# Performance work log

Hardware: AMD Instinct MI355X
Metric: run time of the kernel (lower is better)

Reference implementation:

```python
import jax, jax.numpy as jnp
import numpy as np

N_NODES = 100000
NEG_SLOPE = 0.2  # PyG GATConv default


def gat_conv(x, src, dst, W, a_src, a_dst, n_nodes):
    """One PyG-style GATConv (with self-loops already appended to src/dst).
    x: [N, Fin], W: [Fin, H*C], a_src/a_dst: [H, C]. Returns [N, H, C]."""
    H, C = a_src.shape
    h = (x @ W).reshape(-1, H, C)                      # [N, H, C]
    s_src = jnp.einsum('nhc,hc->nh', h, a_src)         # [N, H]
    s_dst = jnp.einsum('nhc,hc->nh', h, a_dst)         # [N, H]
    e = jax.nn.leaky_relu(s_src[src] + s_dst[dst], NEG_SLOPE)  # [E, H]
    # segment softmax over incoming edges of each destination node
    e_max = jax.ops.segment_max(e, dst, num_segments=n_nodes)  # [N, H]
    e_exp = jnp.exp(e - e_max[dst])
    denom = jax.ops.segment_sum(e_exp, dst, num_segments=n_nodes)
    alpha = e_exp / (denom[dst] + 1e-16)               # [E, H]
    msg = h[src] * alpha[:, :, None]                   # [E, H, C]
    return jax.ops.segment_sum(msg, dst, num_segments=n_nodes)  # [N, H, C]


def setup_inputs() -> dict:
    key = jax.random.key(0)
    ks = jax.random.split(key, 10)
    in_dim, hidden, heads, out_dim = 128, 32, 4, 32
    N, E = N_NODES, 1600000
    x = jax.random.normal(ks[0], (N, in_dim), dtype=jnp.float32)
    edge_index = jax.random.randint(ks[1], (2, E), 0, N, dtype=jnp.int64)
    s = 0.1
    return {
        'x': x,
        'edge_index': edge_index,
        'W1': s * jax.random.normal(ks[2], (in_dim, heads * hidden), dtype=jnp.float32),
        'a_src1': s * jax.random.normal(ks[3], (heads, hidden), dtype=jnp.float32),
        'a_dst1': s * jax.random.normal(ks[4], (heads, hidden), dtype=jnp.float32),
        'b1': jnp.zeros((heads * hidden,), dtype=jnp.float32),
        'W2': s * jax.random.normal(ks[5], (heads * hidden, out_dim), dtype=jnp.float32),
        'a_src2': s * jax.random.normal(ks[6], (1, out_dim), dtype=jnp.float32),
        'a_dst2': s * jax.random.normal(ks[7], (1, out_dim), dtype=jnp.float32),
        'b2': jnp.zeros((out_dim,), dtype=jnp.float32),
    }


def reference(x, edge_index, W1, a_src1, a_dst1, b1, W2, a_src2, a_dst2, b2):
    N = x.shape[0]
    loops = jnp.arange(N, dtype=edge_index.dtype)
    src = jnp.concatenate([edge_index[0], loops])  # PyG adds self-loops
    dst = jnp.concatenate([edge_index[1], loops])
    h1 = gat_conv(x, src, dst, W1, a_src1, a_dst1, N)      # [N, H, C]
    h1 = jax.nn.elu(h1.reshape(N, -1) + b1)                # concat heads + bias, elu
    h2 = gat_conv(h1, src, dst, W2, a_src2, a_dst2, N)     # [N, 1, out]
    return h2.mean(axis=1) + b2                            # concat=False -> mean over heads
```

## Files before the change

kernel.cpp:

```cpp
#include <hip/hip_runtime.h>
#include <hip/hip_bf16.h>

#define NEG 0.2f
#define BK_SHIFT 9
#define BK_CAP 9216

typedef short short8 __attribute__((ext_vector_type(8)));
typedef float f32x4 __attribute__((ext_vector_type(4)));

__device__ __forceinline__ float lrelu(float x){ return x > 0.f ? x : NEG * x; }
__device__ __forceinline__ float elu_fast(float x){ return x > 0.f ? x : __expf(x) - 1.f; }
__device__ __forceinline__ unsigned short f2bf(float f){
  unsigned int u = __float_as_uint(f);
  unsigned int r = u + 0x7fffu + ((u >> 16) & 1u);
  return (unsigned short)(r >> 16);
}
__device__ __forceinline__ float bf2f(unsigned short u){
  return __uint_as_float(((unsigned int)u) << 16);
}
__device__ __forceinline__ float2 bfu2(unsigned int v){
  float2 r;
  r.x = __uint_as_float(v << 16);
  r.y = __uint_as_float(v & 0xffff0000u);
  return r;
}

#define EB_SRC_MASK 0x7fffffu

__global__ __launch_bounds__(512) void k_binA_packW(
    const int* __restrict__ src, const int* __restrict__ dst, int E,
    int* __restrict__ gcursor, unsigned int* __restrict__ ebuf,
    const float* __restrict__ W, unsigned short* __restrict__ Wp,
    const float* __restrict__ W2, unsigned short* __restrict__ Wp2, int nA){
  __shared__ int hist[256];
  __shared__ int base[256];
  int t = threadIdx.x;
  int bid = blockIdx.x;
  if (bid >= nA){
    int idx = (bid - nA) * 512 + t;
    if (idx < 16384){
      int n = idx >> 7, k = idx & 127;
      Wp[n * 128 + k] = f2bf(W[(size_t)k * 128 + n]);
    } else {
      int i2 = idx - 16384;
      int n = i2 >> 7, k = i2 & 127;
      Wp2[n * 128 + k] = f2bf(W2[(size_t)k * 32 + n]);
    }
    return;
  }
  if (t < 256) hist[t] = 0;
  __syncthreads();
  int e0 = bid * 4096;
  int dsr[8], ssr[8];
  #pragma unroll
  for (int j = 0; j < 8; j++){
    int e = e0 + j * 512 + t;
    if (e < E){
      dsr[j] = dst[e]; ssr[j] = src[e];
      atomicAdd(&hist[dsr[j] >> BK_SHIFT], 1);
    } else dsr[j] = -1;
  }
  __syncthreads();
  if (t < 256){
    int cnt = hist[t];
    if (cnt > 0) base[t] = atomicAdd(&gcursor[t], cnt);
    hist[t] = 0;
  }
  __syncthreads();
  #pragma unroll
  for (int j = 0; j < 8; j++){
    if (dsr[j] >= 0){
      int d = dsr[j]; int b = d >> BK_SHIFT;
      int loc = atomicAdd(&hist[b], 1);
      unsigned int dloc = (unsigned int)(d & ((1 << BK_SHIFT) - 1));
      ebuf[(size_t)b * BK_CAP + base[b] + loc] = (unsigned int)ssr[j] | (dloc << 23);
    }
  }
}

__global__ __launch_bounds__(256, 3) void k_csrC_gemm1(
    const unsigned int* __restrict__ ebuf, const int* __restrict__ gcount,
    int* __restrict__ rowp, int* __restrict__ csr, int N, int NBK, int total,
    const float* __restrict__ x, const unsigned short* __restrict__ Wp,
    const float* __restrict__ a_src, const float* __restrict__ a_dst,
    unsigned short* __restrict__ h_bf, float* __restrict__ ss, float* __restrict__ sd){
  __shared__ __align__(16) unsigned short Wt[128 * 136];
  __shared__ __align__(16) unsigned short Xb[64 * 136];
  int t = threadIdx.x;

  if (blockIdx.x < (unsigned)NBK){
    int* hist = (int*)Wt;
    int* psum = hist + 512;
    int* bsum = psum + 256;
    int b = blockIdx.x;
    int nbase = b << BK_SHIFT;
    int cnt = gcount[b];
    const unsigned int* eb = ebuf + (size_t)b * BK_CAP;
    hist[t] = 0; hist[t + 256] = 0;
    int bv = 0;
    {
      int nodes = 0;
      if (t < NBK){ int nb = N - (t << BK_SHIFT); nodes = nb > 512 ? 512 : nb; bv = gcount[t] + nodes; }
      bsum[t] = bv;
    }
    __syncthreads();
    for (int off = 1; off < 256; off <<= 1){
      int xv = (t >= off) ? bsum[t - off] : 0;
      __syncthreads();
      bsum[t] += xv;
      __syncthreads();
    }
    for (int i = t; i < cnt; i += 256)
      atomicAdd(&hist[eb[i] >> 23], 1);
    __syncthreads();
    int v0 = hist[2 * t], v1 = hist[2 * t + 1];
    int ps = v0 + v1;
    psum[t] = ps;
    __syncthreads();
    for (int off = 1; off < 256; off <<= 1){
      int xv = (t >= off) ? psum[t - off] : 0;
      __syncthreads();
      psum[t] += xv;
      __syncthreads();
    }
    {
      int eo = psum[t] - ps;
      int bb = (b == 0) ? 0 : bsum[b - 1];
      int n0 = 2 * t, n1 = 2 * t + 1;
      int r0 = bb + eo + n0;
      int r1 = bb + eo + v0 + n1;
      if (nbase + n0 < N) rowp[nbase + n0] = r0;
      if (nbase + n1 < N) rowp[nbase + n1] = r1;
      hist[n0] = r0; hist[n1] = r1;
    }
    if (b == 0 && t == 0) rowp[N] = total;
    __syncthreads();
    for (int i = t; i < cnt; i += 256){
      unsigned int e = eb[i];
      int pos = atomicAdd(&hist[e >> 23], 1);
      csr[pos] = (int)(e & EB_SRC_MASK);
    }
    __syncthreads();
    {
      int n0 = 2 * t, n1 = 2 * t + 1;
      if (nbase + n0 < N) csr[hist[n0]] = nbase + n0;
      if (nbase + n1 < N) csr[hist[n1]] = nbase + n1;
    }
    return;
  }

  int rb = (blockIdx.x - NBK) * 64;

  #pragma unroll
  for (int j = 0; j < 8; j++){
    int fi = j * 256 + t;
    int n = fi >> 4, ch = fi & 15;
    *(uint4*)&Wt[n * 136 + ch * 8] = *(const uint4*)&Wp[n * 128 + ch * 8];
  }
  #pragma unroll
  for (int j = 0; j < 8; j++){
    int fi = j * 256 + t;
    int row = fi >> 5, k4 = (fi & 31) * 4;
    int gr = rb + row;
    float4 v = make_float4(0.f, 0.f, 0.f, 0.f);
    if (gr < N) v = *(const float4*)&x[(size_t)gr * 128 + k4];
    uint2 pk;
    pk.x = ((unsigned)f2bf(v.y) << 16) | f2bf(v.x);
    pk.y = ((unsigned)f2bf(v.w) << 16) | f2bf(v.z);
    *(uint2*)&Xb[row * 136 + k4] = pk;
  }
  __syncthreads();

  int w = t >> 6, l = t & 63;
  int m = l & 15, quad = l >> 4;
  f32x4 acc[8];
  #pragma unroll
  for (int ct = 0; ct < 8; ct++) acc[ct] = (f32x4){0.f, 0.f, 0.f, 0.f};

  #pragma unroll
  for (int kc = 0; kc < 4; kc++){
    short8 a = *(const short8*)&Xb[(w * 16 + m) * 136 + kc * 32 + quad * 8];
    #pragma unroll
    for (int ct = 0; ct < 8; ct++){
      short8 bfr = *(const short8*)&Wt[(ct * 16 + m) * 136 + kc * 32 + quad * 8];
      acc[ct] = __builtin_amdgcn_mfma_f32_16x16x32_bf16(a, bfr, acc[ct], 0, 0, 0);
    }
  }

  float as[8], ad[8];
  #pragma unroll
  for (int ct = 0; ct < 8; ct++){ as[ct] = a_src[ct * 16 + m]; ad[ct] = a_dst[ct * 16 + m]; }

  #pragma unroll
  for (int reg = 0; reg < 4; reg++){
    int gr = rb + w * 16 + quad * 4 + reg;
    bool ok = gr < N;
    if (ok){
      #pragma unroll
      for (int ct = 0; ct < 8; ct++)
        h_bf[(size_t)gr * 128 + ct * 16 + m] = f2bf(acc[ct][reg]);
    }
    #pragma unroll
    for (int hh = 0; hh < 4; hh++){
      float pss = acc[2*hh][reg] * as[2*hh] + acc[2*hh+1][reg] * as[2*hh+1];
      float pd = acc[2*hh][reg] * ad[2*hh] + acc[2*hh+1][reg] * ad[2*hh+1];
      pss += __shfl_xor(pss, 1, 16); pss += __shfl_xor(pss, 2, 16);
      pss += __shfl_xor(pss, 4, 16); pss += __shfl_xor(pss, 8, 16);
      pd += __shfl_xor(pd, 1, 16); pd += __shfl_xor(pd, 2, 16);
      pd += __shfl_xor(pd, 4, 16); pd += __shfl_xor(pd, 8, 16);
      if (m == 0 && ok){ ss[(size_t)gr * 4 + hh] = pss; sd[(size_t)gr * 4 + hh] = pd; }
    }
  }
}

__global__ __launch_bounds__(256) void k_agg1(
    const int* __restrict__ row_ptr, const int* __restrict__ csr_src,
    const float* __restrict__ ss, const float* __restrict__ sdst,
    const unsigned short* __restrict__ hb,
    unsigned int* __restrict__ out1_bf, int N){
  int n = blockIdx.x * 4 + (threadIdx.x >> 6);
  if (n >= N) return;
  int l = threadIdx.x & 63;
  int q  = (l & 7) + ((l >> 5) << 3);
  int hh = (l >> 3) & 3;
  int slot = l >> 4;
  int c = l & 15;
  int hd = c >> 2;
  float sdw = sdst[(size_t)n * 4 + hh];
  int beg = row_ptr[n], end = row_ptr[n + 1];

  float acc[8] = {0.f,0.f,0.f,0.f,0.f,0.f,0.f,0.f};
  float swacc = 0.f;

  int e = beg;
  int remaining = end - beg;
  int qc = q < remaining ? q : 0;
  int sj = csr_src[e + qc];
  float sv = ss[(size_t)sj * 4 + hh];

  while (remaining > 0){
    int cur = remaining > 16 ? 16 : remaining;
    float wv = (q < cur) ? __expf(lrelu(sv + sdw)) : 0.f;
    swacc += wv;
    int sjc = sj;
    int rn = remaining - 16;
    if (rn > 0){
      int qn = q < rn ? q : 0;
      sj = csr_src[e + 16 + qn];
      sv = ss[(size_t)sj * 4 + hh];
    }
    #pragma unroll
    for (int p = 0; p < 4; p++){
      int base_p = ((p & 1) << 2) + ((p >> 1) << 3);
      if (base_p < cur){
        int sl = ((p & 1) << 2) + slot + ((p >> 1) << 5);
        int s  = __shfl(sjc, sl, 64);
        float w = __shfl(wv, sl + (hd << 3), 64);
        uint4 u = *(const uint4*)&hb[(size_t)s * 128 + (c << 3)];
        float2 f0 = bfu2(u.x), f1 = bfu2(u.y), f2 = bfu2(u.z), f3 = bfu2(u.w);
        acc[0] += w * f0.x; acc[1] += w * f0.y;
        acc[2] += w * f1.x; acc[3] += w * f1.y;
        acc[4] += w * f2.x; acc[5] += w * f2.y;
        acc[6] += w * f3.x; acc[7] += w * f3.y;
      }
    }
    e += 16; remaining = rn;
  }

  #pragma unroll
  for (int i = 0; i < 8; i++){
    acc[i] += __shfl_xor(acc[i], 16, 64);
    acc[i] += __shfl_xor(acc[i], 32, 64);
  }
  swacc += __shfl_xor(swacc, 1, 64);
  swacc += __shfl_xor(swacc, 2, 64);
  swacc += __shfl_xor(swacc, 4, 64);
  swacc += __shfl_xor(swacc, 32, 64);
  float sw = __shfl(swacc, hd << 3, 64);
  float inv = 1.f / (sw + 1e-16f);
  if (slot == 0){
    unsigned int o0 = ((unsigned)f2bf(acc[1] * inv) << 16) | f2bf(acc[0] * inv);
    unsigned int o1 = ((unsigned)f2bf(acc[3] * inv) << 16) | f2bf(acc[2] * inv);
    unsigned int o2 = ((unsigned)f2bf(acc[5] * inv) << 16) | f2bf(acc[4] * inv);
    unsigned int o3 = ((unsigned)f2bf(acc[7] * inv) << 16) | f2bf(acc[6] * inv);
    uint4 o; o.x = o0; o.y = o1; o.z = o2; o.w = o3;
    *(uint4*)&out1_bf[(size_t)n * 64 + (c << 2)] = o;
  }
}

__global__ __launch_bounds__(256) void k_gemm2m(
    const unsigned int* __restrict__ out1_bf, const float* __restrict__ b1,
    const unsigned short* __restrict__ Wp2,
    const float* __restrict__ a_src, const float* __restrict__ a_dst,
    unsigned short* __restrict__ h2_bf, float* __restrict__ ss2, float* __restrict__ sd2, int N){
  __shared__ __align__(16) unsigned short Wt[32 * 136];
  __shared__ __align__(16) unsigned short Xb[64 * 136];
  int t = threadIdx.x;
  int rb = blockIdx.x * 64;

  #pragma unroll
  for (int j = 0; j < 2; j++){
    int fi = j * 256 + t;
    int n = fi >> 4, ch = fi & 15;
    *(uint4*)&Wt[n * 136 + ch * 8] = *(const uint4*)&Wp2[n * 128 + ch * 8];
  }
  #pragma unroll
  for (int j = 0; j < 4; j++){
    int fi = j * 256 + t;
    int row = fi >> 4, q = fi & 15;
    int gr = rb + row;
    uint4 o = make_uint4(0u, 0u, 0u, 0u);
    if (gr < N){
      uint4 u = *(const uint4*)&out1_bf[(size_t)gr * 64 + q * 4];
      float4 bva = *(const float4*)&b1[q * 8];
      float4 bvb = *(const float4*)&b1[q * 8 + 4];
      float v0 = elu_fast(bf2f((unsigned short)(u.x & 0xffff)) + bva.x);
      float v1 = elu_fast(bf2f((unsigned short)(u.x >> 16))    + bva.y);
      float v2 = elu_fast(bf2f((unsigned short)(u.y & 0xffff)) + bva.z);
      float v3 = elu_fast(bf2f((unsigned short)(u.y >> 16))    + bva.w);
      float v4 = elu_fast(bf2f((unsigned short)(u.z & 0xffff)) + bvb.x);
      float v5 = elu_fast(bf2f((unsigned short)(u.z >> 16))    + bvb.y);
      float v6 = elu_fast(bf2f((unsigned short)(u.w & 0xffff)) + bvb.z);
      float v7 = elu_fast(bf2f((unsigned short)(u.w >> 16))    + bvb.w);
      o.x = ((unsigned)f2bf(v1) << 16) | f2bf(v0);
      o.y = ((unsigned)f2bf(v3) << 16) | f2bf(v2);
      o.z = ((unsigned)f2bf(v5) << 16) | f2bf(v4);
      o.w = ((unsigned)f2bf(v7) << 16) | f2bf(v6);
    }
    *(uint4*)&Xb[row * 136 + q * 8] = o;
  }
  __syncthreads();

  int w = t >> 6, l = t & 63;
  int m = l & 15, quad = l >> 4;
  f32x4 acc[2];
  acc[0] = (f32x4){0.f, 0.f, 0.f, 0.f};
  acc[1] = (f32x4){0.f, 0.f, 0.f, 0.f};

  #pragma unroll
  for (int kc = 0; kc < 4; kc++){
    short8 a = *(const short8*)&Xb[(w * 16 + m) * 136 + kc * 32 + quad * 8];
    #pragma unroll
    for (int ct = 0; ct < 2; ct++){
      short8 bfr = *(const short8*)&Wt[(ct * 16 + m) * 136 + kc * 32 + quad * 8];
      acc[ct] = __builtin_amdgcn_mfma_f32_16x16x32_bf16(a, bfr, acc[ct], 0, 0, 0);
    }
  }

  float as0 = a_src[m], as1 = a_src[16 + m];
  float ad0 = a_dst[m], ad1 = a_dst[16 + m];

  #pragma unroll
  for (int reg = 0; reg < 4; reg++){
    int gr = rb + w * 16 + quad * 4 + reg;
    bool ok = gr < N;
    if (ok){
      h2_bf[(size_t)gr * 32 + m]      = f2bf(acc[0][reg]);
      h2_bf[(size_t)gr * 32 + 16 + m] = f2bf(acc[1][reg]);
    }
    float ps = acc[0][reg] * as0 + acc[1][reg] * as1;
    float pd = acc[0][reg] * ad0 + acc[1][reg] * ad1;
    ps += __shfl_xor(ps, 1, 16); ps += __shfl_xor(ps, 2, 16);
    ps += __shfl_xor(ps, 4, 16); ps += __shfl_xor(ps, 8, 16);
    pd += __shfl_xor(pd, 1, 16); pd += __shfl_xor(pd, 2, 16);
    pd += __shfl_xor(pd, 4, 16); pd += __shfl_xor(pd, 8, 16);
    if (m == 0 && ok){ ss2[gr] = ps; sd2[gr] = pd; }
  }
}

__global__ __launch_bounds__(256) void k_agg2(
    const int* __restrict__ row_ptr, const int* __restrict__ csr_src,
    const float* __restrict__ ss2, const float* __restrict__ sd2,
    const unsigned short* __restrict__ h2bf, const float* __restrict__ b2,
    float* __restrict__ out, int N){
  int n = blockIdx.x * 4 + (threadIdx.x >> 6);
  if (n >= N) return;
  int l = threadIdx.x & 63;
  int q = l & 15;
  int slot = l >> 2;
  int ch4 = l & 3;
  float sdv = sd2[n];
  int beg = row_ptr[n], end = row_ptr[n + 1];

  float acc[8] = {0.f,0.f,0.f,0.f,0.f,0.f,0.f,0.f};
  float swacc = 0.f;

  int e = beg;
  int remaining = end - beg;
  int qc = q < remaining ? q : 0;
  int sj = csr_src[e + qc];
  float sv = ss2[sj];

  while (remaining > 0){
    int cur = remaining > 16 ? 16 : remaining;
    float wv = (q < cur) ? __expf(lrelu(sv + sdv)) : 0.f;
    swacc += wv;
    int sjc = sj; float wvc = wv;
    int rn = remaining - 16;
    if (rn > 0){
      int qn = q < rn ? q : 0;
      sj = csr_src[e + 16 + qn];
      sv = ss2[sj];
    }
    {
      int s  = __shfl(sjc, slot, 64);
      float w = __shfl(wvc, slot, 64);
      if (slot < cur){
        uint4 u = *(const uint4*)&h2bf[(size_t)s * 32 + (ch4 << 3)];
        float2 f0 = bfu2(u.x), f1 = bfu2(u.y), f2 = bfu2(u.z), f3 = bfu2(u.w);
        acc[0] += w * f0.x; acc[1] += w * f0.y;
        acc[2] += w * f1.x; acc[3] += w * f1.y;
        acc[4] += w * f2.x; acc[5] += w * f2.y;
        acc[6] += w * f3.x; acc[7] += w * f3.y;
      }
    }
    e += 16; remaining = rn;
  }

  #pragma unroll
  for (int i = 0; i < 8; i++){
    acc[i] += __shfl_xor(acc[i], 4, 64);
    acc[i] += __shfl_xor(acc[i], 8, 64);
    acc[i] += __shfl_xor(acc[i], 16, 64);
    acc[i] += __shfl_xor(acc[i], 32, 64);
  }
  swacc += __shfl_xor(swacc, 1, 64);
  swacc += __shfl_xor(swacc, 2, 64);
  swacc += __shfl_xor(swacc, 4, 64);
  swacc += __shfl_xor(swacc, 8, 64);
  float inv = 1.f / (swacc + 1e-16f);
  if (slot == 0){
    float4 bva = *(const float4*)&b2[(ch4 << 3)];
    float4 bvb = *(const float4*)&b2[(ch4 << 3) + 4];
    float4 oa, ob;
    oa.x = acc[0] * inv + bva.x; oa.y = acc[1] * inv + bva.y;
    oa.z = acc[2] * inv + bva.z; oa.w = acc[3] * inv + bva.w;
    ob.x = acc[4] * inv + bvb.x; ob.y = acc[5] * inv + bvb.y;
    ob.z = acc[6] * inv + bvb.z; ob.w = acc[7] * inv + bvb.w;
    *(float4*)&out[(size_t)n * 32 + (ch4 << 3)] = oa;
    *(float4*)&out[(size_t)n * 32 + (ch4 << 3) + 4] = ob;
  }
}

extern "C" void kernel_launch(void* const* d_in, const int* in_sizes, int n_in,
                              void* d_out, int out_size, void* d_ws, size_t ws_size,
                              hipStream_t stream) {
  const float* x      = (const float*)d_in[0];
  const int*   ei     = (const int*)  d_in[1];
  const float* W1     = (const float*)d_in[2];
  const float* a_src1 = (const float*)d_in[3];
  const float* a_dst1 = (const float*)d_in[4];
  const float* b1     = (const float*)d_in[5];
  const float* W2     = (const float*)d_in[6];
  const float* a_src2 = (const float*)d_in[7];
  const float* a_dst2 = (const float*)d_in[8];
  const float* b2     = (const float*)d_in[9];
  float* out = (float*)d_out;

  int N = in_sizes[0] / 128;
  int E = in_sizes[1] / 2;
  const int* srcp = ei;
  const int* dstp = ei + E;
  int total = E + N;
  int NBK = (N + 511) >> 9;

  char* p = (char*)d_ws;
  auto alloc = [&](size_t bytes) -> void* {
    void* r = (void*)p; p += (bytes + 255) & ~(size_t)255; return r;
  };
  unsigned short* h_bf    = (unsigned short*)alloc((size_t)N * 128 * 2);
  unsigned int*   out1_bf = (unsigned int*)alloc((size_t)N * 64 * 4);
  unsigned short* h2_bf   = (unsigned short*)alloc((size_t)N * 32 * 2);
  unsigned short* Wp      = (unsigned short*)alloc(128 * 128 * 2);
  unsigned short* Wp2     = (unsigned short*)alloc(32 * 128 * 2);
  float* ss1  = (float*)alloc((size_t)N * 4 * 4);
  float* sd1  = (float*)alloc((size_t)N * 4 * 4);
  float* ss2  = (float*)alloc((size_t)N * 4);
  float* sd2  = (float*)alloc((size_t)N * 4);
  int* rowp   = (int*)alloc((size_t)(N + 1) * 4);
  int* csr    = (int*)alloc((size_t)total * 4);
  int* gcur   = (int*)alloc(256 * 4);
  unsigned int* ebuf = (unsigned int*)out1_bf;
  (void)ws_size; (void)n_in; (void)out_size;

  int nA = (E + 4095) / 4096;
  int nG = (N + 63) / 64;

  hipMemsetAsync(gcur, 0, 256 * 4, stream);
  k_binA_packW<<<nA + 40, 512, 0, stream>>>(srcp, dstp, E, gcur, ebuf, W1, Wp, W2, Wp2, nA);
  k_csrC_gemm1<<<NBK + nG, 256, 0, stream>>>(ebuf, gcur, rowp, csr, N, NBK, total,
                                             x, Wp, a_src1, a_dst1, h_bf, ss1, sd1);
  k_agg1<<<(N + 3) / 4, 256, 0, stream>>>(rowp, csr, ss1, sd1, h_bf, out1_bf, N);
  k_gemm2m<<<nG, 256, 0, stream>>>(out1_bf, b1, Wp2, a_src2, a_dst2, h2_bf, ss2, sd2, N);
  k_agg2<<<(N + 3) / 4, 256, 0, stream>>>(rowp, csr, ss2, sd2, h2_bf, b2, out, N);
}
```

Measured before the change: 292.2 us.

## Fuse bias+ELU into agg1 epilogue, widen gemm2 tile and agg2 edge batch

Moves the layer-1 bias add and ELU from the gemm2 load stage into the agg1 epilogue, so the intermediate is stored already activated. This removes per-element conversion work from k_gemm2m and also skips a bf16 round before the ELU. k_gemm2m now processes 128 rows per block, reusing each weight fragment across two row groups. k_agg2 handles 32 edges per loop iteration instead of 16 to expose more memory parallelism. The costs are twice the LDS per gemm2 block and more registers in agg2.

Result: no change. 291.9 us (-0.1%).

```diff
diff --git a/kernel.cpp b/kernel.cpp
--- a/kernel.cpp
+++ b/kernel.cpp
@@ -216,8 +216,8 @@
 __global__ __launch_bounds__(256) void k_agg1(
     const int* __restrict__ row_ptr, const int* __restrict__ csr_src,
     const float* __restrict__ ss, const float* __restrict__ sdst,
-    const unsigned short* __restrict__ hb,
-    unsigned int* __restrict__ out1_bf, int N){
+    const unsigned short* __restrict__ hb, const float* __restrict__ b1,
+    unsigned int* __restrict__ y_bf, int N){
   int n = blockIdx.x * 4 + (threadIdx.x >> 6);
   if (n >= N) return;
   int l = threadIdx.x & 63;
@@ -279,24 +279,34 @@
   float sw = __shfl(swacc, hd << 3, 64);
   float inv = 1.f / (sw + 1e-16f);
   if (slot == 0){
-    unsigned int o0 = ((unsigned)f2bf(acc[1] * inv) << 16) | f2bf(acc[0] * inv);
-    unsigned int o1 = ((unsigned)f2bf(acc[3] * inv) << 16) | f2bf(acc[2] * inv);
-    unsigned int o2 = ((unsigned)f2bf(acc[5] * inv) << 16) | f2bf(acc[4] * inv);
-    unsigned int o3 = ((unsigned)f2bf(acc[7] * inv) << 16) | f2bf(acc[6] * inv);
+    float4 bva = *(const float4*)&b1[c * 8];
+    float4 bvb = *(const float4*)&b1[c * 8 + 4];
+    float y0 = elu_fast(acc[0] * inv + bva.x);
+    float y1 = elu_fast(acc[1] * inv + bva.y);
+    float y2 = elu_fast(acc[2] * inv + bva.z);
+    float y3 = elu_fast(acc[3] * inv + bva.w);
+    float y4 = elu_fast(acc[4] * inv + bvb.x);
+    float y5 = elu_fast(acc[5] * inv + bvb.y);
+    float y6 = elu_fast(acc[6] * inv + bvb.z);
+    float y7 = elu_fast(acc[7] * inv + bvb.w);
+    unsigned int o0 = ((unsigned)f2bf(y1) << 16) | f2bf(y0);
+    unsigned int o1 = ((unsigned)f2bf(y3) << 16) | f2bf(y2);
+    unsigned int o2 = ((unsigned)f2bf(y5) << 16) | f2bf(y4);
+    unsigned int o3 = ((unsigned)f2bf(y7) << 16) | f2bf(y6);
     uint4 o; o.x = o0; o.y = o1; o.z = o2; o.w = o3;
-    *(uint4*)&out1_bf[(size_t)n * 64 + (c << 2)] = o;
+    *(uint4*)&y_bf[(size_t)n * 64 + (c << 2)] = o;
   }
 }
 
 __global__ __launch_bounds__(256) void k_gemm2m(
-    const unsigned int* __restrict__ out1_bf, const float* __restrict__ b1,
+    const unsigned int* __restrict__ y_bf,
     const unsigned short* __restrict__ Wp2,
     const float* __restrict__ a_src, const float* __restrict__ a_dst,
     unsigned short* __restrict__ h2_bf, float* __restrict__ ss2, float* __restrict__ sd2, int N){
   __shared__ __align__(16) unsigned short Wt[32 * 136];
-  __shared__ __align__(16) unsigned short Xb[64 * 136];
+  __shared__ __align__(16) unsigned short Xb[128 * 136];
   int t = threadIdx.x;
-  int rb = blockIdx.x * 64;
+  int rb = blockIdx.x * 128;
 
   #pragma unroll
   for (int j = 0; j < 2; j++){
@@ -305,45 +315,35 @@
     *(uint4*)&Wt[n * 136 + ch * 8] = *(const uint4*)&Wp2[n * 128 + ch * 8];
   }
   #pragma unroll
-  for (int j = 0; j < 4; j++){
+  for (int j = 0; j < 8; j++){
     int fi = j * 256 + t;
-    int row = fi >> 4, q = fi & 15;
+    int row = fi >> 4, qq = fi & 15;
     int gr = rb + row;
     uint4 o = make_uint4(0u, 0u, 0u, 0u);
-    if (gr < N){
-      uint4 u = *(const uint4*)&out1_bf[(size_t)gr * 64 + q * 4];
-      float4 bva = *(const float4*)&b1[q * 8];
-      float4 bvb = *(const float4*)&b1[q * 8 + 4];
-      float v0 = elu_fast(bf2f((unsigned short)(u.x & 0xffff)) + bva.x);
-      float v1 = elu_fast(bf2f((unsigned short)(u.x >> 16))    + bva.y);
-      float v2 = elu_fast(bf2f((unsigned short)(u.y & 0xffff)) + bva.z);
-      float v3 = elu_fast(bf2f((unsigned short)(u.y >> 16))    + bva.w);
-      float v4 = elu_fast(bf2f((unsigned short)(u.z & 0xffff)) + bvb.x);
-      float v5 = elu_fast(bf2f((unsigned short)(u.z >> 16))    + bvb.y);
-      float v6 = elu_fast(bf2f((unsigned short)(u.w & 0xffff)) + bvb.z);
-      float v7 = elu_fast(bf2f((unsigned short)(u.w >> 16))    + bvb.w);
-      o.x = ((unsigned)f2bf(v1) << 16) | f2bf(v0);
-      o.y = ((unsigned)f2bf(v3) << 16) | f2bf(v2);
-      o.z = ((unsigned)f2bf(v5) << 16) | f2bf(v4);
-      o.w = ((unsigned)f2bf(v7) << 16) | f2bf(v6);
-    }
-    *(uint4*)&Xb[row * 136 + q * 8] = o;
+    if (gr < N) o = *(const uint4*)&y_bf[(size_t)gr * 64 + qq * 4];
+    *(uint4*)&Xb[row * 136 + qq * 8] = o;
   }
   __syncthreads();
 
   int w = t >> 6, l = t & 63;
   int m = l & 15, quad = l >> 4;
-  f32x4 acc[2];
-  acc[0] = (f32x4){0.f, 0.f, 0.f, 0.f};
-  acc[1] = (f32x4){0.f, 0.f, 0.f, 0.f};
+  f32x4 acc[2][2];
+  #pragma unroll
+  for (int rg = 0; rg < 2; rg++){
+    acc[rg][0] = (f32x4){0.f, 0.f, 0.f, 0.f};
+    acc[rg][1] = (f32x4){0.f, 0.f, 0.f, 0.f};
+  }
 
   #pragma unroll
   for (int kc = 0; kc < 4; kc++){
-    short8 a = *(const short8*)&Xb[(w * 16 + m) * 136 + kc * 32 + quad * 8];
     #pragma unroll
     for (int ct = 0; ct < 2; ct++){
       short8 bfr = *(const short8*)&Wt[(ct * 16 + m) * 136 + kc * 32 + quad * 8];
-      acc[ct] = __builtin_amdgcn_mfma_f32_16x16x32_bf16(a, bfr, acc[ct], 0, 0, 0);
+      #pragma unroll
+      for (int rg = 0; rg < 2; rg++){
+        short8 a = *(const short8*)&Xb[(rg * 64 + w * 16 + m) * 136 + kc * 32 + quad * 8];
+        acc[rg][ct] = __builtin_amdgcn_mfma_f32_16x16x32_bf16(a, bfr, acc[rg][ct], 0, 0, 0);
+      }
     }
   }
 
@@ -351,20 +351,23 @@
   float ad0 = a_dst[m], ad1 = a_dst[16 + m];
 
   #pragma unroll
-  for (int reg = 0; reg < 4; reg++){
-    int gr = rb + w * 16 + quad * 4 + reg;
-    bool ok = gr < N;
-    if (ok){
-      h2_bf[(size_t)gr * 32 + m]      = f2bf(acc[0][reg]);
-      h2_bf[(size_t)gr * 32 + 16 + m] = f2bf(acc[1][reg]);
-    }
-    float ps = acc[0][reg] * as0 + acc[1][reg] * as1;
-    float pd = acc[0][reg] * ad0 + acc[1][reg] * ad1;
-    ps += __shfl_xor(ps, 1, 16); ps += __shfl_xor(ps, 2, 16);
-    ps += __shfl_xor(ps, 4, 16); ps += __shfl_xor(ps, 8, 16);
-    pd += __shfl_xor(pd, 1, 16); pd += __shfl_xor(pd, 2, 16);
-    pd += __shfl_xor(pd, 4, 16); pd += __shfl_xor(pd, 8, 16);
-    if (m == 0 && ok){ ss2[gr] = ps; sd2[gr] = pd; }
+  for (int rg = 0; rg < 2; rg++){
+    #pragma unroll
+    for (int reg = 0; reg < 4; reg++){
+      int gr = rb + rg * 64 + w * 16 + quad * 4 + reg;
+      bool ok = gr < N;
+      if (ok){
+        h2_bf[(size_t)gr * 32 + m]      = f2bf(acc[rg][0][reg]);
+        h2_bf[(size_t)gr * 32 + 16 + m] = f2bf(acc[rg][1][reg]);
+      }
+      float ps = acc[rg][0][reg] * as0 + acc[rg][1][reg] * as1;
+      float pd = acc[rg][0][reg] * ad0 + acc[rg][1][reg] * ad1;
+      ps += __shfl_xor(ps, 1, 16); ps += __shfl_xor(ps, 2, 16);
+      ps += __shfl_xor(ps, 4, 16); ps += __shfl_xor(ps, 8, 16);
+      pd += __shfl_xor(pd, 1, 16); pd += __shfl_xor(pd, 2, 16);
+      pd += __shfl_xor(pd, 4, 16); pd += __shfl_xor(pd, 8, 16);
+      if (m == 0 && ok){ ss2[gr] = ps; sd2[gr] = pd; }
+    }
   }
 }
 
@@ -376,7 +379,7 @@
   int n = blockIdx.x * 4 + (threadIdx.x >> 6);
   if (n >= N) return;
   int l = threadIdx.x & 63;
-  int q = l & 15;
+  int q = l & 31;
   int slot = l >> 2;
   int ch4 = l & 3;
   float sdv = sd2[n];
@@ -392,14 +395,14 @@
   float sv = ss2[sj];
 
   while (remaining > 0){
-    int cur = remaining > 16 ? 16 : remaining;
+    int cur = remaining > 32 ? 32 : remaining;
     float wv = (q < cur) ? __expf(lrelu(sv + sdv)) : 0.f;
     swacc += wv;
     int sjc = sj; float wvc = wv;
-    int rn = remaining - 16;
+    int rn = remaining - 32;
     if (rn > 0){
       int qn = q < rn ? q : 0;
-      sj = csr_src[e + 16 + qn];
+      sj = csr_src[e + 32 + qn];
       sv = ss2[sj];
     }
     {
@@ -414,7 +417,19 @@
         acc[6] += w * f3.x; acc[7] += w * f3.y;
       }
     }
-    e += 16; remaining = rn;
+    if (cur > 16){
+      int s  = __shfl(sjc, 16 + slot, 64);
+      float w = __shfl(wvc, 16 + slot, 64);
+      if (16 + slot < cur){
+        uint4 u = *(const uint4*)&h2bf[(size_t)s * 32 + (ch4 << 3)];
+        float2 f0 = bfu2(u.x), f1 = bfu2(u.y), f2 = bfu2(u.z), f3 = bfu2(u.w);
+        acc[0] += w * f0.x; acc[1] += w * f0.y;
+        acc[2] += w * f1.x; acc[3] += w * f1.y;
+        acc[4] += w * f2.x; acc[5] += w * f2.y;
+        acc[6] += w * f3.x; acc[7] += w * f3.y;
+      }
+    }
+    e += 32; remaining = rn;
   }
 
   #pragma unroll
@@ -428,6 +443,7 @@
   swacc += __shfl_xor(swacc, 2, 64);
   swacc += __shfl_xor(swacc, 4, 64);
   swacc += __shfl_xor(swacc, 8, 64);
+  swacc += __shfl_xor(swacc, 16, 64);
   float inv = 1.f / (swacc + 1e-16f);
   if (slot == 0){
     float4 bva = *(const float4*)&b2[(ch4 << 3)];
@@ -469,7 +485,7 @@
     void* r = (void*)p; p += (bytes + 255) & ~(size_t)255; return r;
   };
   unsigned short* h_bf    = (unsigned short*)alloc((size_t)N * 128 * 2);
-  unsigned int*   out1_bf = (unsigned int*)alloc((size_t)N * 64 * 4);
+  unsigned int*   y_bf    = (unsigned int*)alloc((size_t)N * 64 * 4);
   unsigned short* h2_bf   = (unsigned short*)alloc((size_t)N * 32 * 2);
   unsigned short* Wp      = (unsigned short*)alloc(128 * 128 * 2);
   unsigned short* Wp2     = (unsigned short*)alloc(32 * 128 * 2);
@@ -480,17 +496,18 @@
   int* rowp   = (int*)alloc((size_t)(N + 1) * 4);
   int* csr    = (int*)alloc((size_t)total * 4);
   int* gcur   = (int*)alloc(256 * 4);
-  unsigned int* ebuf = (unsigned int*)out1_bf;
+  unsigned int* ebuf = (unsigned int*)y_bf;
   (void)ws_size; (void)n_in; (void)out_size;
 
   int nA = (E + 4095) / 4096;
   int nG = (N + 63) / 64;
+  int nG2 = (N + 127) / 128;
 
   hipMemsetAsync(gcur, 0, 256 * 4, stream);
   k_binA_packW<<<nA + 40, 512, 0, stream>>>(srcp, dstp, E, gcur, ebuf, W1, Wp, W2, Wp2, nA);
   k_csrC_gemm1<<<NBK + nG, 256, 0, stream>>>(ebuf, gcur, rowp, csr, N, NBK, total,
                                              x, Wp, a_src1, a_dst1, h_bf, ss1, sd1);
-  k_agg1<<<(N + 3) / 4, 256, 0, stream>>>(rowp, csr, ss1, sd1, h_bf, out1_bf, N);
-  k_gemm2m<<<nG, 256, 0, stream>>>(out1_bf, b1, Wp2, a_src2, a_dst2, h2_bf, ss2, sd2, N);
+  k_agg1<<<(N + 3) / 4, 256, 0, stream>>>(rowp, csr, ss1, sd1, h_bf, b1, y_bf, N);
+  k_gemm2m<<<nG2, 256, 0, stream>>>(y_bf, Wp2, a_src2, a_dst2, h2_bf, ss2, sd2, N);
   k_agg2<<<(N + 3) / 4, 256, 0, stream>>>(rowp, csr, ss2, sd2, h2_bf, b2, out, N);
 }
```
